# Kernel optimization log

Measured on AMD Instinct MI355X. Metric: run time of the kernel, lower is better.

## Reference

```python
import jax, jax.numpy as jnp
import numpy as np

H = 64  # LSTM hidden size
IN = 5  # input feature size
N_ACTIONS = 3


def _init_params(key):
    ks = jax.random.split(key, 16)
    def u(k, shape, fan_in):
        b = 1.0 / np.sqrt(fan_in)
        return jax.random.uniform(k, shape, jnp.float32, -b, b)
    p = {}
    # PyTorch LSTM params: gate order i, f, g, o stacked along dim 0
    p['W_ih'] = u(ks[0], (4 * H, IN), H)
    p['W_hh'] = u(ks[1], (4 * H, H), H)
    p['b_ih'] = u(ks[2], (4 * H,), H)
    p['b_hh'] = u(ks[3], (4 * H,), H)
    p['W1'] = u(ks[4], (256, 64), 64); p['b1'] = u(ks[5], (256,), 64)
    p['W2'] = u(ks[6], (64, 256), 256); p['b2'] = u(ks[7], (64,), 256)
    p['W3'] = u(ks[8], (32, 64), 64); p['b3'] = u(ks[9], (32,), 64)
    p['W4'] = u(ks[10], (16, 32), 32); p['b4'] = u(ks[11], (16,), 32)
    p['Wh'] = u(ks[12], (N_ACTIONS, 16), 16); p['bh'] = u(ks[13], (N_ACTIONS,), 16)
    return p


def setup_inputs() -> dict:
    key = jax.random.key(0)
    k_x, k_h, k_c, k_p = jax.random.split(key, 4)
    B = 262144
    inp = {
        'x': jax.random.normal(k_x, (2, B, IN), jnp.float32),
        'h0': jax.random.normal(k_h, (B, H), jnp.float32),
        'c0': jax.random.normal(k_c, (B, H), jnp.float32),
    }
    inp.update(_init_params(k_p))
    return inp


def _lstm_step(x_t, h, c, W_ih, W_hh, b_ih, b_hh):
    # gates: [B, 4H], PyTorch order i, f, g, o
    gates = x_t @ W_ih.T + h @ W_hh.T + (b_ih + b_hh)
    i, f, g, o = jnp.split(gates, 4, axis=-1)
    i = jax.nn.sigmoid(i)
    f = jax.nn.sigmoid(f)
    g = jnp.tanh(g)
    o = jax.nn.sigmoid(o)
    c = f * c + i * g
    h = o * jnp.tanh(c)
    return h, c


def reference(x, h0, c0, W_ih, W_hh, b_ih, b_hh, W1, b1, W2, b2, W3, b3, W4, b4, Wh, bh):
    # 2-step LSTM (seq_len hard-coded to 2 in the torch module)
    h, c = h0, c0
    for t in range(2):
        h, c = _lstm_step(x[t], h, c, W_ih, W_hh, b_ih, b_hh)
    # take last timestep output, relu, then 4-layer MLP + head
    z = jax.nn.relu(h)
    z = jax.nn.relu(z @ W1.T + b1)
    z = jax.nn.relu(z @ W2.T + b2)
    z = jax.nn.relu(z @ W3.T + b3)
    z = jax.nn.relu(z @ W4.T + b4)
    return z @ Wh.T + bh
```

## Files before the change

kernel.cpp:

```cpp
#include <hip/hip_runtime.h>

typedef _Float16 f16;
typedef _Float16 f16x4 __attribute__((ext_vector_type(4)));
typedef _Float16 f16x8 __attribute__((ext_vector_type(8)));
typedef float    f32x4 __attribute__((ext_vector_type(4)));

#define MFMA(A,B,C) __builtin_amdgcn_mfma_f32_16x16x32_f16((A),(B),(C),0,0,0)

__device__ __forceinline__ float sig2(float y) {
    return __builtin_amdgcn_rcpf(1.0f + __builtin_amdgcn_exp2f(-y));
}

constexpr float L2E  = 1.4426950408889634f;
constexpr float L2E2 = 2.8853900817779268f;

constexpr int STR = 72;

constexpr int OFF_WG = 0;
constexpr int OFF_W1 = 18432;
constexpr int OFF_W2 = 34816;
constexpr int OFF_W3 = 51200;
constexpr int OFF_W4 = 53248;
constexpr int OFF_WH = 53760;
constexpr int WS_TOT = 54272;

__global__ void wprep(const float* __restrict__ Wih, const float* __restrict__ Whh,
                      const float* __restrict__ bih, const float* __restrict__ bhh,
                      const float* __restrict__ w1p, const float* __restrict__ w2p,
                      const float* __restrict__ w3p, const float* __restrict__ w4p,
                      const float* __restrict__ whp, f16* __restrict__ ws) {
    int idx = blockIdx.x * 256 + threadIdx.x;
    if (idx >= WS_TOT) return;
    float v = 0.0f;
    if (idx < OFF_W1) {
        int r = idx, kb = r >> 11, n = (r >> 3) & 255, j = r & 7;
        float sc = (n >= 128 && n < 192) ? L2E2 : L2E;
        if (kb < 8)      v = Whh[n * 64 + kb * 8 + j];
        else if (j < 5)  v = Wih[n * 5 + j];
        else if (j == 5) v = bih[n] + bhh[n];
        v *= sc;
    } else if (idx < OFF_W2) {
        int r = idx - OFF_W1, kt = r >> 11, n = (r >> 3) & 255, j = r & 7;
        v = w1p[n * 64 + kt * 8 + j];
    } else if (idx < OFF_W3) {
        int r = idx - OFF_W2, kt = r >> 9, n = (r >> 3) & 63, j = r & 7;
        v = w2p[n * 256 + kt * 8 + j];
    } else if (idx < OFF_W4) {
        int r = idx - OFF_W3, kt = r >> 8, n = (r >> 3) & 31, j = r & 7;
        v = w3p[n * 64 + kt * 8 + j];
    } else if (idx < OFF_WH) {
        int r = idx - OFF_W4, kt = r >> 7, n = (r >> 3) & 15, j = r & 7;
        v = w4p[n * 32 + kt * 8 + j];
    } else {
        int r = idx - OFF_WH, kt = r >> 7, n = (r >> 3) & 15, j = r & 7;
        int k = kt * 8 + j;
        v = (k < 16 && n < 3) ? whp[n * 16 + k] : 0.0f;
    }
    ws[idx] = (f16)v;
}

__global__ __launch_bounds__(512, 4)
void lstmdqn_v16(const float* __restrict__ xg,  const float* __restrict__ h0g,
                 const float* __restrict__ c0g,
                 const f16* __restrict__ ws,
                 const float* __restrict__ b1p, const float* __restrict__ b2p,
                 const float* __restrict__ b3p, const float* __restrict__ b4p,
                 const float* __restrict__ bhp,
                 float* __restrict__ out, int Bsz, int nt16) {
    __shared__ f16 sAB[128 * STR];
    __shared__ f16 sWG[9 * 256 * 8];
    __shared__ f16 sZL[2560];
    __shared__ float sBB[372];

    const int tid  = threadIdx.x;
    const int w    = tid >> 6, l = tid & 63;
    const int lrow = l & 15, hi = l >> 4;
    const int wrow = w * 16;

    {
        const int4* src = (const int4*)(ws + OFF_WG);
        int4* dst = (int4*)sWG;
        for (int i = tid; i < 18432 / 8; i += 512) dst[i] = src[i];
    }
    for (int i = tid; i < 2560; i += 512) sZL[i] = (f16)0.0f;
    if (tid < 256) sBB[tid] = b1p[tid];
    if (tid < 64)  sBB[256 + tid] = b2p[tid];
    if (tid < 32)  sBB[320 + tid] = b3p[tid];
    if (tid < 16)  sBB[352 + tid] = b4p[tid];
    if (tid < 3)   sBB[368 + tid] = bhp[tid];
    for (int i = tid; i < 128 * 3; i += 512) {
        int r = i / 3, c = 69 + (i - 3 * r);
        sAB[r * STR + c] = (f16)(c == 69 ? 1.0f : 0.0f);
    }
    __syncthreads();

    const f16* pA  = &sAB[(wrow + lrow) * STR + hi * 8];
    const f16* pA2 = (hi == 0) ? &sAB[(wrow + lrow) * STR + 64] : &sZL[l * 8];
    const f16* pWG  = &sWG[(hi * 256 + lrow) * 8];
    const f16* pWG2 = (hi == 0) ? &sWG[8 * 2048 + lrow * 8] : &sZL[l * 8];
    const int rwb = (wrow + 4 * hi) * STR + lrow;

    float4 hpre0 = {0,0,0,0}, hpre1 = {0,0,0,0}, hpre2 = {0,0,0,0}, hpre3 = {0,0,0,0};
    float4 x0pre = {0,0,0,0}, x1pre = {0,0,0,0};
    {
        int t0 = blockIdx.x * 8 + w;
        if (t0 < nt16) {
            const float* hp = h0g + (size_t)t0 * 16 * 64;
            hpre0 = *(const float4*)(hp + 0 * 256 + l * 4);
            hpre1 = *(const float4*)(hp + 1 * 256 + l * 4);
            hpre2 = *(const float4*)(hp + 2 * 256 + l * 4);
            hpre3 = *(const float4*)(hp + 3 * 256 + l * 4);
            if (l < 20) {
                x0pre = *(const float4*)(xg + (size_t)t0 * 80 + 4 * l);
                x1pre = *(const float4*)(xg + (size_t)Bsz * 5 + (size_t)t0 * 80 + 4 * l);
            }
        }
    }

    #pragma unroll 1
    for (int tile = blockIdx.x * 8 + w; tile < nt16; tile += (gridDim.x << 3)) {
        const int rbase = tile * 16;

        uintptr_t uW1 = (uintptr_t)(ws + OFF_W1 + (hi * 256 + lrow) * 8);
        uintptr_t uW2 = (uintptr_t)(ws + OFF_W2 + (hi * 64 + lrow) * 8);
        uintptr_t uW3 = (uintptr_t)(ws + OFF_W3 + (hi * 32 + lrow) * 8);
        uintptr_t uW4 = (uintptr_t)(ws + OFF_W4 + (hi * 16 + lrow) * 8);
        uintptr_t uWh = (uintptr_t)(ws + OFF_WH + (hi * 16 + lrow) * 8);
        asm volatile("" : "+v"(uW1), "+v"(uW2), "+v"(uW3), "+v"(uW4), "+v"(uWh));
        const f16* gW1 = (const f16*)uW1;
        const f16* gW2 = (const f16*)uW2;
        const f16* gW3 = (const f16*)uW3;
        const f16* gW4 = (const f16*)uW4;
        const f16* gWh = (const f16*)uWh;

        {
            int r0 = wrow + (l >> 4);
            int col = (4 * l) & 63;
            f16x4 h0v = { (f16)hpre0.x, (f16)hpre0.y, (f16)hpre0.z, (f16)hpre0.w };
            f16x4 h1v = { (f16)hpre1.x, (f16)hpre1.y, (f16)hpre1.z, (f16)hpre1.w };
            f16x4 h2v = { (f16)hpre2.x, (f16)hpre2.y, (f16)hpre2.z, (f16)hpre2.w };
            f16x4 h3v = { (f16)hpre3.x, (f16)hpre3.y, (f16)hpre3.z, (f16)hpre3.w };
            *(f16x4*)&sAB[(r0 +  0) * STR + col] = h0v;
            *(f16x4*)&sAB[(r0 +  4) * STR + col] = h1v;
            *(f16x4*)&sAB[(r0 +  8) * STR + col] = h2v;
            *(f16x4*)&sAB[(r0 + 12) * STR + col] = h3v;
        }
        if (l < 20) {
            float vv[4] = { x0pre.x, x0pre.y, x0pre.z, x0pre.w };
            #pragma unroll
            for (int e = 0; e < 4; ++e) {
                int idx = 4 * l + e, r = idx / 5, ft = idx - 5 * r;
                sAB[(wrow + r) * STR + 64 + ft] = (f16)vv[e];
            }
        }
        float creg[4][4];
        #pragma unroll
        for (int gq = 0; gq < 4; ++gq)
            #pragma unroll
            for (int q = 0; q < 4; ++q)
                creg[gq][q] = c0g[(size_t)(rbase + 4 * hi + q) * 64 + gq * 16 + lrow];

        #pragma unroll
        for (int t = 0; t < 2; ++t) {
            f16x8 af0 = *(const f16x8*)&pA[0];
            f16x8 af1 = *(const f16x8*)&pA[32];
            f16x8 af2 = *(const f16x8*)pA2;
            if (t == 0 && l < 20) {
                float vv[4] = { x1pre.x, x1pre.y, x1pre.z, x1pre.w };
                #pragma unroll
                for (int e = 0; e < 4; ++e) {
                    int idx = 4 * l + e, r = idx / 5, ft = idx - 5 * r;
                    sAB[(wrow + r) * STR + 64 + ft] = (f16)vv[e];
                }
            }
            #pragma unroll
            for (int gq = 0; gq < 4; ++gq) {
                f32x4 ag[4];
                #pragma unroll
                for (int g4 = 0; g4 < 4; ++g4) {
                    int ct = gq + 4 * g4;
                    f16x8 b0 = *(const f16x8*)&pWG[ct * 128];
                    f16x8 b1 = *(const f16x8*)&pWG[8192 + ct * 128];
                    f16x8 b2 = *(const f16x8*)&pWG2[ct * 128];
                    f32x4 a = { 0.f, 0.f, 0.f, 0.f };
                    a = MFMA(af0, b0, a);
                    a = MFMA(af1, b1, a);
                    a = MFMA(af2, b2, a);
                    ag[g4] = a;
                }
                #pragma unroll
                for (int q = 0; q < 4; ++q) {
                    float iv = sig2(ag[0][q]);
                    float fv = sig2(ag[1][q]);
                    float gv = 2.0f * sig2(ag[2][q]) - 1.0f;
                    float ov = sig2(ag[3][q]);
                    float c  = fv * creg[gq][q] + iv * gv;
                    creg[gq][q] = c;
                    float tc = 2.0f * sig2(L2E2 * c) - 1.0f;
                    float h  = ov * tc;
                    if (t == 1) h = fmaxf(h, 0.0f);
                    sAB[rwb + q * STR + gq * 16] = (f16)h;
                }
            }
        }

        {
            int nxt = tile + (gridDim.x << 3);
            if (nxt < nt16) {
                const float* hp = h0g + (size_t)nxt * 16 * 64;
                hpre0 = *(const float4*)(hp + 0 * 256 + l * 4);
                hpre1 = *(const float4*)(hp + 1 * 256 + l * 4);
                hpre2 = *(const float4*)(hp + 2 * 256 + l * 4);
                hpre3 = *(const float4*)(hp + 3 * 256 + l * 4);
                if (l < 20) {
                    x0pre = *(const float4*)(xg + (size_t)nxt * 80 + 4 * l);
                    x1pre = *(const float4*)(xg + (size_t)Bsz * 5 + (size_t)nxt * 80 + 4 * l);
                }
            }
        }

        f16x8 za0 = *(const f16x8*)&pA[0];
        f16x8 za1 = *(const f16x8*)&pA[32];
        f32x4 acc2[4];
        #pragma unroll
        for (int c2 = 0; c2 < 4; ++c2)
            acc2[c2] = (f32x4){ 0.f, 0.f, 0.f, 0.f };
        #pragma unroll
        for (int cc = 0; cc < 4; ++cc) {
            #pragma unroll
            for (int ctl = 0; ctl < 4; ++ctl) {
                int ct = cc * 4 + ctl;
                f16x8 b0 = *(const f16x8*)&gW1[ct * 128];
                f16x8 b1 = *(const f16x8*)&gW1[8192 + ct * 128];
                float bv = sBB[ct * 16 + lrow];
                f32x4 a = { 0.f, 0.f, 0.f, 0.f };
                a = MFMA(za0, b0, a);
                a = MFMA(za1, b1, a);
                #pragma unroll
                for (int q = 0; q < 4; ++q) {
                    float v = fmaxf(a[q] + bv, 0.0f);
                    sAB[rwb + q * STR + ctl * 16] = (f16)v;
                }
            }
            f16x8 ca0 = *(const f16x8*)&pA[0];
            f16x8 ca1 = *(const f16x8*)&pA[32];
            #pragma unroll
            for (int ct2 = 0; ct2 < 4; ++ct2) {
                f16x8 wb0 = *(const f16x8*)&gW2[cc * 4096 + ct2 * 128];
                f16x8 wb1 = *(const f16x8*)&gW2[cc * 4096 + 2048 + ct2 * 128];
                acc2[ct2] = MFMA(ca0, wb0, acc2[ct2]);
                acc2[ct2] = MFMA(ca1, wb1, acc2[ct2]);
            }
        }
        #pragma unroll
        for (int ct2 = 0; ct2 < 4; ++ct2) {
            float bv = sBB[256 + ct2 * 16 + lrow];
            #pragma unroll
            for (int q = 0; q < 4; ++q) {
                float v = fmaxf(acc2[ct2][q] + bv, 0.0f);
                sAB[rwb + q * STR + ct2 * 16] = (f16)v;
            }
        }
        {
            f16x8 a30 = *(const f16x8*)&pA[0];
            f16x8 a31 = *(const f16x8*)&pA[32];
            #pragma unroll
            for (int ctt = 0; ctt < 2; ++ctt) {
                f16x8 c0f = *(const f16x8*)&gW3[ctt * 128];
                f16x8 c1f = *(const f16x8*)&gW3[1024 + ctt * 128];
                float bv = sBB[320 + ctt * 16 + lrow];
                f32x4 a = { 0.f, 0.f, 0.f, 0.f };
                a = MFMA(a30, c0f, a);
                a = MFMA(a31, c1f, a);
                #pragma unroll
                for (int q = 0; q < 4; ++q) {
                    float v = fmaxf(a[q] + bv, 0.0f);
                    sAB[rwb + q * STR + ctt * 16] = (f16)v;
                }
            }
        }
        {
            f16x8 wb4 = *(const f16x8*)gW4;
            float bv = sBB[352 + lrow];
            f16x8 a4 = *(const f16x8*)&pA[0];
            f32x4 a = { 0.f, 0.f, 0.f, 0.f };
            a = MFMA(a4, wb4, a);
            #pragma unroll
            for (int q = 0; q < 4; ++q) {
                float v = fmaxf(a[q] + bv, 0.0f);
                sAB[rwb + q * STR + 32] = (f16)v;
            }
        }
        {
            f16x8 wbh = *(const f16x8*)gWh;
            f16x8 ah = *(const f16x8*)&pA[32];
            f32x4 a = { 0.f, 0.f, 0.f, 0.f };
            a = MFMA(ah, wbh, a);
            if (lrow < 3) {
                float bv = sBB[368 + lrow];
                #pragma unroll
                for (int q = 0; q < 4; ++q)
                    out[(size_t)(rbase + 4 * hi + q) * 3 + lrow] = a[q] + bv;
            }
        }
    }
}

extern "C" void kernel_launch(void* const* d_in, const int* in_sizes, int n_in,
                              void* d_out, int out_size, void* d_ws, size_t ws_size,
                              hipStream_t stream) {
    const float* x   = (const float*)d_in[0];
    const float* h0  = (const float*)d_in[1];
    const float* c0  = (const float*)d_in[2];
    const float* Wih = (const float*)d_in[3];
    const float* Whh = (const float*)d_in[4];
    const float* bih = (const float*)d_in[5];
    const float* bhh = (const float*)d_in[6];
    const float* w1  = (const float*)d_in[7];
    const float* b1  = (const float*)d_in[8];
    const float* w2  = (const float*)d_in[9];
    const float* b2  = (const float*)d_in[10];
    const float* w3  = (const float*)d_in[11];
    const float* b3  = (const float*)d_in[12];
    const float* w4  = (const float*)d_in[13];
    const float* b4  = (const float*)d_in[14];
    const float* wh  = (const float*)d_in[15];
    const float* bh  = (const float*)d_in[16];

    int Bsz  = in_sizes[1] / 64;
    int nt16 = Bsz / 16;

    f16* ws = (f16*)d_ws;
    wprep<<<(WS_TOT + 255) / 256, 256, 0, stream>>>(Wih, Whh, bih, bhh,
                                                    w1, w2, w3, w4, wh, ws);
    lstmdqn_v16<<<1024, 512, 0, stream>>>(x, h0, c0, ws, b1, b2, b3, b4, bh,
                                          (float*)d_out, Bsz, nt16);
}
```

Before: 87.57 us.

## Transpose MFMA operand order so each lane owns row-contiguous outputs

Swaps the A and B operands of every MFMA so the accumulator holds a transposed tile, where each lane owns four consecutive columns of one batch row. This lets the c0 load become one float4 per gate quarter instead of scattered scalars, turns the four scalar f16 LDS stores per tile into a single f16x4 store, and reads biases as float4. The head output is written as three contiguous floats per row. The grid is also halved from 1024 to 512 blocks, so each block runs more tile iterations; this trades occupancy and tail balance for less launch and setup cost.

```diff
diff --git a/kernel.cpp b/kernel.cpp
--- a/kernel.cpp
+++ b/kernel.cpp
@@ -60,7 +60,7 @@
 }
 
 __global__ __launch_bounds__(512, 4)
-void lstmdqn_v16(const float* __restrict__ xg,  const float* __restrict__ h0g,
+void lstmdqn_v17(const float* __restrict__ xg,  const float* __restrict__ h0g,
                  const float* __restrict__ c0g,
                  const f16* __restrict__ ws,
                  const float* __restrict__ b1p, const float* __restrict__ b2p,
@@ -70,7 +70,7 @@
     __shared__ f16 sAB[128 * STR];
     __shared__ f16 sWG[9 * 256 * 8];
     __shared__ f16 sZL[2560];
-    __shared__ float sBB[372];
+    __shared__ __align__(16) float sBB[372];
 
     const int tid  = threadIdx.x;
     const int w    = tid >> 6, l = tid & 63;
@@ -88,6 +88,7 @@
     if (tid < 32)  sBB[320 + tid] = b3p[tid];
     if (tid < 16)  sBB[352 + tid] = b4p[tid];
     if (tid < 3)   sBB[368 + tid] = bhp[tid];
+    if (tid == 3)  sBB[371] = 0.0f;
     for (int i = tid; i < 128 * 3; i += 512) {
         int r = i / 3, c = 69 + (i - 3 * r);
         sAB[r * STR + c] = (f16)(c == 69 ? 1.0f : 0.0f);
@@ -98,7 +99,7 @@
     const f16* pA2 = (hi == 0) ? &sAB[(wrow + lrow) * STR + 64] : &sZL[l * 8];
     const f16* pWG  = &sWG[(hi * 256 + lrow) * 8];
     const f16* pWG2 = (hi == 0) ? &sWG[8 * 2048 + lrow * 8] : &sZL[l * 8];
-    const int rwb = (wrow + 4 * hi) * STR + lrow;
+    const int rwbT = (wrow + lrow) * STR + 4 * hi;
 
     float4 hpre0 = {0,0,0,0}, hpre1 = {0,0,0,0}, hpre2 = {0,0,0,0}, hpre3 = {0,0,0,0};
     float4 x0pre = {0,0,0,0}, x1pre = {0,0,0,0};
@@ -154,11 +155,15 @@
             }
         }
         float creg[4][4];
-        #pragma unroll
-        for (int gq = 0; gq < 4; ++gq)
-            #pragma unroll
-            for (int q = 0; q < 4; ++q)
-                creg[gq][q] = c0g[(size_t)(rbase + 4 * hi + q) * 64 + gq * 16 + lrow];
+        {
+            const float* cp = c0g + (size_t)(rbase + lrow) * 64 + 4 * hi;
+            #pragma unroll
+            for (int gq = 0; gq < 4; ++gq) {
+                float4 cv = *(const float4*)(cp + gq * 16);
+                creg[gq][0] = cv.x; creg[gq][1] = cv.y;
+                creg[gq][2] = cv.z; creg[gq][3] = cv.w;
+            }
+        }
 
         #pragma unroll
         for (int t = 0; t < 2; ++t) {
@@ -183,11 +188,12 @@
                     f16x8 b1 = *(const f16x8*)&pWG[8192 + ct * 128];
                     f16x8 b2 = *(const f16x8*)&pWG2[ct * 128];
                     f32x4 a = { 0.f, 0.f, 0.f, 0.f };
-                    a = MFMA(af0, b0, a);
-                    a = MFMA(af1, b1, a);
-                    a = MFMA(af2, b2, a);
+                    a = MFMA(b0, af0, a);
+                    a = MFMA(b1, af1, a);
+                    a = MFMA(b2, af2, a);
                     ag[g4] = a;
                 }
+                f16 hq[4];
                 #pragma unroll
                 for (int q = 0; q < 4; ++q) {
                     float iv = sig2(ag[0][q]);
@@ -199,8 +205,10 @@
                     float tc = 2.0f * sig2(L2E2 * c) - 1.0f;
                     float h  = ov * tc;
                     if (t == 1) h = fmaxf(h, 0.0f);
-                    sAB[rwb + q * STR + gq * 16] = (f16)h;
+                    hq[q] = (f16)h;
                 }
+                f16x4 hv = { hq[0], hq[1], hq[2], hq[3] };
+                *(f16x4*)&sAB[rwbT + gq * 16] = hv;
             }
         }
 
@@ -232,15 +240,13 @@
                 int ct = cc * 4 + ctl;
                 f16x8 b0 = *(const f16x8*)&gW1[ct * 128];
                 f16x8 b1 = *(const f16x8*)&gW1[8192 + ct * 128];
-                float bv = sBB[ct * 16 + lrow];
+                f32x4 bv = *(const f32x4*)&sBB[ct * 16 + 4 * hi];
                 f32x4 a = { 0.f, 0.f, 0.f, 0.f };
-                a = MFMA(za0, b0, a);
-                a = MFMA(za1, b1, a);
-                #pragma unroll
-                for (int q = 0; q < 4; ++q) {
-                    float v = fmaxf(a[q] + bv, 0.0f);
-                    sAB[rwb + q * STR + ctl * 16] = (f16)v;
-                }
+                a = MFMA(b0, za0, a);
+                a = MFMA(b1, za1, a);
+                f16x4 zv = { (f16)fmaxf(a[0] + bv[0], 0.f), (f16)fmaxf(a[1] + bv[1], 0.f),
+                             (f16)fmaxf(a[2] + bv[2], 0.f), (f16)fmaxf(a[3] + bv[3], 0.f) };
+                *(f16x4*)&sAB[rwbT + ctl * 16] = zv;
             }
             f16x8 ca0 = *(const f16x8*)&pA[0];
             f16x8 ca1 = *(const f16x8*)&pA[32];
@@ -248,18 +254,16 @@
             for (int ct2 = 0; ct2 < 4; ++ct2) {
                 f16x8 wb0 = *(const f16x8*)&gW2[cc * 4096 + ct2 * 128];
                 f16x8 wb1 = *(const f16x8*)&gW2[cc * 4096 + 2048 + ct2 * 128];
-                acc2[ct2] = MFMA(ca0, wb0, acc2[ct2]);
-                acc2[ct2] = MFMA(ca1, wb1, acc2[ct2]);
+                acc2[ct2] = MFMA(wb0, ca0, acc2[ct2]);
+                acc2[ct2] = MFMA(wb1, ca1, acc2[ct2]);
             }
         }
         #pragma unroll
         for (int ct2 = 0; ct2 < 4; ++ct2) {
-            float bv = sBB[256 + ct2 * 16 + lrow];
-            #pragma unroll
-            for (int q = 0; q < 4; ++q) {
-                float v = fmaxf(acc2[ct2][q] + bv, 0.0f);
-                sAB[rwb + q * STR + ct2 * 16] = (f16)v;
-            }
+            f32x4 bv = *(const f32x4*)&sBB[256 + ct2 * 16 + 4 * hi];
+            f16x4 zv = { (f16)fmaxf(acc2[ct2][0] + bv[0], 0.f), (f16)fmaxf(acc2[ct2][1] + bv[1], 0.f),
+                         (f16)fmaxf(acc2[ct2][2] + bv[2], 0.f), (f16)fmaxf(acc2[ct2][3] + bv[3], 0.f) };
+            *(f16x4*)&sAB[rwbT + ct2 * 16] = zv;
         }
         {
             f16x8 a30 = *(const f16x8*)&pA[0];
@@ -268,39 +272,35 @@
             for (int ctt = 0; ctt < 2; ++ctt) {
                 f16x8 c0f = *(const f16x8*)&gW3[ctt * 128];
                 f16x8 c1f = *(const f16x8*)&gW3[1024 + ctt * 128];
-                float bv = sBB[320 + ctt * 16 + lrow];
+                f32x4 bv = *(const f32x4*)&sBB[320 + ctt * 16 + 4 * hi];
                 f32x4 a = { 0.f, 0.f, 0.f, 0.f };
-                a = MFMA(a30, c0f, a);
-                a = MFMA(a31, c1f, a);
-                #pragma unroll
-                for (int q = 0; q < 4; ++q) {
-                    float v = fmaxf(a[q] + bv, 0.0f);
-                    sAB[rwb + q * STR + ctt * 16] = (f16)v;
-                }
+                a = MFMA(c0f, a30, a);
+                a = MFMA(c1f, a31, a);
+                f16x4 zv = { (f16)fmaxf(a[0] + bv[0], 0.f), (f16)fmaxf(a[1] + bv[1], 0.f),
+                             (f16)fmaxf(a[2] + bv[2], 0.f), (f16)fmaxf(a[3] + bv[3], 0.f) };
+                *(f16x4*)&sAB[rwbT + ctt * 16] = zv;
             }
         }
         {
             f16x8 wb4 = *(const f16x8*)gW4;
-            float bv = sBB[352 + lrow];
+            f32x4 bv = *(const f32x4*)&sBB[352 + 4 * hi];
             f16x8 a4 = *(const f16x8*)&pA[0];
             f32x4 a = { 0.f, 0.f, 0.f, 0.f };
-            a = MFMA(a4, wb4, a);
-            #pragma unroll
-            for (int q = 0; q < 4; ++q) {
-                float v = fmaxf(a[q] + bv, 0.0f);
-                sAB[rwb + q * STR + 32] = (f16)v;
-            }
+            a = MFMA(wb4, a4, a);
+            f16x4 zv = { (f16)fmaxf(a[0] + bv[0], 0.f), (f16)fmaxf(a[1] + bv[1], 0.f),
+                         (f16)fmaxf(a[2] + bv[2], 0.f), (f16)fmaxf(a[3] + bv[3], 0.f) };
+            *(f16x4*)&sAB[rwbT + 32] = zv;
         }
         {
             f16x8 wbh = *(const f16x8*)gWh;
             f16x8 ah = *(const f16x8*)&pA[32];
             f32x4 a = { 0.f, 0.f, 0.f, 0.f };
-            a = MFMA(ah, wbh, a);
-            if (lrow < 3) {
-                float bv = sBB[368 + lrow];
-                #pragma unroll
-                for (int q = 0; q < 4; ++q)
-                    out[(size_t)(rbase + 4 * hi + q) * 3 + lrow] = a[q] + bv;
+            a = MFMA(wbh, ah, a);
+            if (hi == 0) {
+                float* op = out + (size_t)(rbase + lrow) * 3;
+                op[0] = a[0] + sBB[368];
+                op[1] = a[1] + sBB[369];
+                op[2] = a[2] + sBB[370];
             }
         }
     }
@@ -333,6 +333,6 @@
     f16* ws = (f16*)d_ws;
     wprep<<<(WS_TOT + 255) / 256, 256, 0, stream>>>(Wih, Whh, bih, bhh,
                                                     w1, w2, w3, w4, wh, ws);
-    lstmdqn_v16<<<1024, 512, 0, stream>>>(x, h0, c0, ws, b1, b2, b3, b4, bh,
-                                          (float*)d_out, Bsz, nt16);
+    lstmdqn_v17<<<512, 512, 0, stream>>>(x, h0, c0, ws, b1, b2, b3, b4, bh,
+                                         (float*)d_out, Bsz, nt16);
 }
```

New measurement: 253.2 us. 189% more time.
